# Optimization experiments

Hardware: AMD Instinct MI355X
Metric: run time of the kernel (lower is better)

Reference implementation:

```python
import jax, jax.numpy as jnp
import numpy as np

DEPTH = 16
Q_DIM = 64
V_DIM = 64
BATCH = 2048


def setup_inputs() -> dict:
    key = jax.random.key(0)
    k1, k2, k3 = jax.random.split(key, 3)
    query = jax.random.normal(k1, (BATCH, Q_DIM), dtype=jnp.float32)
    # internal-node keys: (2^depth - 1) nodes, each with 2 child keys of dim q_dim
    tree_key = jax.random.normal(k2, (2 ** DEPTH - 1, 2, Q_DIM), dtype=jnp.float32)
    # leaf values: 2^depth leaves of dim v_dim
    tree_value = jax.random.normal(k3, (2 ** DEPTH, V_DIM), dtype=jnp.float32)
    return {"query": query, "tree_key": tree_key, "tree_value": tree_value}


def _tree_attention(query, tree_key, tree_value, depth):
    # Hierarchical softmax attention over a complete binary tree.
    # At each internal node, a 2-way softmax over <query, child_key> logits
    # splits probability mass between left/right subtrees; leaf weight is the
    # product of probabilities along its root-to-leaf path.
    B = query.shape[0]
    probs = jnp.ones((B, 1), dtype=query.dtype)
    start = 0
    for d in range(depth):
        n = 2 ** d  # nodes at this level, stored contiguously at [start, start+n)
        level_keys = tree_key[start:start + n]           # (n, 2, q_dim)
        logits = jnp.einsum('bq,ncq->bnc', query, level_keys)  # (B, n, 2)
        p = jax.nn.softmax(logits, axis=-1)               # (B, n, 2)
        probs = (probs[:, :, None] * p).reshape(B, 2 * n)  # (B, 2n)
        start += n
    # weighted combination of leaf values: (B, 2^depth) @ (2^depth, v_dim)
    return probs @ tree_value


def reference(query, tree_key, tree_value):
    return _tree_attention(query, tree_key, tree_value, DEPTH)
```

## Files before the change

### kernel.cpp

```cpp
#include <hip/hip_runtime.h>

#define LOG2E 1.44269504088896f

typedef _Float16 half8  __attribute__((ext_vector_type(8)));
typedef _Float16 half4v __attribute__((ext_vector_type(4)));
typedef float    floatx4 __attribute__((ext_vector_type(4)));

#define WS_KD   0u
#define WS_VT   8388608u
#define WS_PART 16777216u

__device__ __forceinline__ floatx4 mfma16(half8 a, half8 b, floatx4 c) {
    return __builtin_amdgcn_mfma_f32_16x16x32_f16(a, b, c, 0, 0, 0);
}

__device__ __forceinline__ float sigmf(float d) {
    return __builtin_amdgcn_rcpf(1.0f + __builtin_amdgcn_exp2f(d * (-LOG2E)));
}

__device__ __forceinline__ void gl_lds16(const void* gsrc, void* ldst) {
    __builtin_amdgcn_global_load_lds(
        (const __attribute__((address_space(1))) unsigned int*)gsrc,
        (__attribute__((address_space(3))) unsigned int*)ldst,
        16, 0, 0);
}

__global__ __launch_bounds__(256)
void k_prep(const float* __restrict__ tkey, const float* __restrict__ tval,
            char* __restrict__ ws)
{
    __shared__ _Float16 sT[64 * 72];
    const int bid = blockIdx.x, tid = threadIdx.x;

    {
        const int l = tid >> 2, part = tid & 3;
        const floatx4* vp = (const floatx4*)(tval + ((size_t)bid * 64 + l) * 64) + part * 4;
        #pragma unroll
        for (int t4 = 0; t4 < 4; ++t4) {
            floatx4 f = vp[t4];
            #pragma unroll
            for (int e = 0; e < 4; ++e)
                sT[(part * 16 + t4 * 4 + e) * 72 + l] = (_Float16)f[e];
        }
    }
    __syncthreads();
    {
        const int v = tid >> 2, q4 = tid & 3;
        half8 x0 = *(const half8*)(sT + v * 72 + 16 * q4);
        half8 x1 = *(const half8*)(sT + v * 72 + 16 * q4 + 8);
        char* base = ws + WS_VT + (size_t)bid * 8192 + v * 128;
        const int swz = (v & 7) << 4;
        *(half8*)(base + ((q4 * 32)      ^ swz)) = x0;
        *(half8*)(base + ((q4 * 32 + 16) ^ swz)) = x1;
    }

    #pragma unroll
    for (int k = 0; k < 2; ++k) {
        const int gt  = bid * 512 + k * 256 + tid;
        const int rid = gt >> 3, part = gt & 7;
        const int s = rid >> 6, j = rid & 63;
        const size_t dst = (size_t)WS_KD + (size_t)s * 8192 + j * 128 + ((part * 16) ^ ((j & 7) << 4));
        half8 out;
        if (j < 63) {
            const int u = j + 1;
            const int f = 31 - __builtin_clz(u);
            const int i = u - (1 << f);
            const int gidx = ((1 << (10 + f)) - 1) + (s << f) + i;
            const floatx4* kp = (const floatx4*)(tkey + (size_t)gidx * 128) + part * 2;
            floatx4 a0 = kp[0], a1 = kp[1];
            floatx4 b0 = kp[16], b1 = kp[17];
            #pragma unroll
            for (int e = 0; e < 4; ++e) {
                out[e]     = (_Float16)(a0[e] - b0[e]);
                out[4 + e] = (_Float16)(a1[e] - b1[e]);
            }
        } else {
            #pragma unroll
            for (int e = 0; e < 8; ++e) out[e] = (_Float16)0.f;
        }
        *(half8*)(ws + dst) = out;
    }
}

__global__ __launch_bounds__(256, 2)
void k_main(const float* __restrict__ q,
            const float* __restrict__ tkey,
            const char* __restrict__ wsc,
            _Float16* __restrict__ pout)
{
    __shared__ _Float16 sA[256 * 64];
    __shared__ _Float16 sPT[256 * 72];
    __shared__ _Float16 sB[64 * 64];

    const int tid  = threadIdx.x;
    const int w    = tid >> 6;
    const int lane = tid & 63;
    const int lm   = lane & 15;
    const int quad = lane >> 4;
    const int xcd  = blockIdx.x & 7;
    const int ix   = blockIdx.x >> 3;
    const int g    = xcd * 8 + (ix >> 3);
    const int tb   = ix & 7;

    {
        const int j = tid >> 3, part = tid & 7;
        int gidx = -1;
        if (j < 6) {
            gidx = (1 << j) - 1 + (g >> (6 - j));
        } else if (j < 21) {
            const int u = j - 5;
            const int e = 31 - __builtin_clz(u);
            const int i = u - (1 << e);
            gidx = ((1 << (6 + e)) - 1) + (g << e) + i;
        }
        half8 out;
        if (gidx >= 0) {
            const floatx4* kp = (const floatx4*)(tkey + (size_t)gidx * 128) + part * 2;
            floatx4 a0 = kp[0], a1 = kp[1];
            floatx4 b0 = kp[16], b1 = kp[17];
            #pragma unroll
            for (int e = 0; e < 4; ++e) {
                out[e]     = (_Float16)(a0[e] - b0[e]);
                out[4 + e] = (_Float16)(a1[e] - b1[e]);
            }
        } else {
            #pragma unroll
            for (int e = 0; e < 8; ++e) out[e] = (_Float16)0.f;
        }
        *(half8*)(sB + j * 64 + ((part * 8) ^ ((j & 7) << 3))) = out;
    }

    {
        const int r = tid;
        const floatx4* qp = (const floatx4*)(q + (size_t)(tb * 256 + r) * 64);
        const int sw = (r & 7) << 3;
        #pragma unroll
        for (int t4 = 0; t4 < 8; ++t4) {
            floatx4 f0 = qp[2 * t4], f1 = qp[2 * t4 + 1];
            half8 hv;
            #pragma unroll
            for (int e = 0; e < 4; ++e) { hv[e] = (_Float16)f0[e]; hv[4 + e] = (_Float16)f1[e]; }
            *(half8*)(sA + r * 64 + ((t4 * 8) ^ sw)) = hv;
        }
    }
    __syncthreads();

    half8 qA[4][2];
    #pragma unroll
    for (int m = 0; m < 4; ++m) {
        const int rA = 64 * w + 16 * m + lm;
        const int sw = (lm & 7) << 3;
        #pragma unroll
        for (int kt = 0; kt < 2; ++kt)
            qA[m][kt] = *(const half8*)(sA + rA * 64 + ((kt * 32 + quad * 8) ^ sw));
    }

    {
        #pragma unroll
        for (int nt = 0; nt < 2; ++nt) {
            const int row = 16 * nt + lm;
            const int sw = (lm & 7) << 3;
            half8 bf0 = *(const half8*)(sB + row * 64 + ((quad * 8) ^ sw));
            half8 bf1 = *(const half8*)(sB + row * 64 + ((32 + quad * 8) ^ sw));
            floatx4 acc[4];
            #pragma unroll
            for (int m = 0; m < 4; ++m) {
                acc[m][0] = 0.f; acc[m][1] = 0.f; acc[m][2] = 0.f; acc[m][3] = 0.f;
                acc[m] = mfma16(bf0, qA[m][0], acc[m]);
                acc[m] = mfma16(bf1, qA[m][1], acc[m]);
            }
            #pragma unroll
            for (int m = 0; m < 4; ++m) {
                half4v ph;
                #pragma unroll
                for (int r = 0; r < 4; ++r) ph[r] = (_Float16)sigmf(acc[m][r]);
                *(half4v*)(sPT + (64 * w + 16 * m + lm) * 72 + 16 * nt + 4 * quad) = ph;
            }
        }
    }
    __syncthreads();

    const int bb = tid;
    float pref = 1.f;
    #pragma unroll
    for (int d = 0; d < 6; ++d) {
        float pv = (float)sPT[bb * 72 + d];
        pref *= ((g >> (5 - d)) & 1) ? (1.f - pv) : pv;
    }
    const float p6    = (float)sPT[bb * 72 + 6];
    const float p7_0  = (float)sPT[bb * 72 + 7],  p7_1  = (float)sPT[bb * 72 + 8];
    const float p9_0  = (float)sPT[bb * 72 + 9],  p9_1  = (float)sPT[bb * 72 + 10];
    const float p9_2  = (float)sPT[bb * 72 + 11], p9_3  = (float)sPT[bb * 72 + 12];
    const float p13_0 = (float)sPT[bb * 72 + 13], p13_1 = (float)sPT[bb * 72 + 14];
    const float p13_2 = (float)sPT[bb * 72 + 15], p13_3 = (float)sPT[bb * 72 + 16];
    const float p13_4 = (float)sPT[bb * 72 + 17], p13_5 = (float)sPT[bb * 72 + 18];
    const float p13_6 = (float)sPT[bb * 72 + 19], p13_7 = (float)sPT[bb * 72 + 20];

    floatx4 O[4][4];
    #pragma unroll
    for (int m = 0; m < 4; ++m)
        #pragma unroll
        for (int nt = 0; nt < 4; ++nt) { O[m][nt][0]=0.f; O[m][nt][1]=0.f; O[m][nt][2]=0.f; O[m][nt][3]=0.f; }

    for (int sl = 0; sl < 16; ++sl) {
        const int s = (g << 4) + sl;

        {
            const char* kd = wsc + WS_KD + (size_t)s * 8192;
            gl_lds16(kd + w * 2048 +        lane * 16, sB + w * 1024);
            gl_lds16(kd + w * 2048 + 1024 + lane * 16, sB + w * 1024 + 512);
        }
        half8 vf[4][2];
        {
            const char* vt = wsc + WS_VT + (size_t)s * 8192;
            #pragma unroll
            for (int nt = 0; nt < 4; ++nt) {
                const int row = 16 * nt + lm;
                const int swz = (lm & 7) << 4;
                #pragma unroll
                for (int kt = 0; kt < 2; ++kt)
                    vf[nt][kt] = *(const half8*)(vt + row * 128 + ((kt * 64 + quad * 16) ^ swz));
            }
        }
        __syncthreads();

        __builtin_amdgcn_s_setprio(1);
        #pragma unroll
        for (int nt = 0; nt < 4; ++nt) {
            const int row = 16 * nt + lm;
            const int sw = (lm & 7) << 3;
            half8 bf0 = *(const half8*)(sB + row * 64 + ((quad * 8) ^ sw));
            half8 bf1 = *(const half8*)(sB + row * 64 + ((32 + quad * 8) ^ sw));
            floatx4 acc[4];
            #pragma unroll
            for (int m = 0; m < 4; ++m) {
                acc[m][0] = 0.f; acc[m][1] = 0.f; acc[m][2] = 0.f; acc[m][3] = 0.f;
                acc[m] = mfma16(bf0, qA[m][0], acc[m]);
                acc[m] = mfma16(bf1, qA[m][1], acc[m]);
            }
            #pragma unroll
            for (int m = 0; m < 4; ++m) {
                half4v ph;
                #pragma unroll
                for (int r = 0; r < 4; ++r) ph[r] = (_Float16)sigmf(acc[m][r]);
                *(half4v*)(sPT + (64 * w + 16 * m + lm) * 72 + 16 * nt + 4 * quad) = ph;
            }
        }
        __builtin_amdgcn_s_setprio(0);
        __syncthreads();

        const int a0 = sl >> 3, a1 = sl >> 2, a2 = sl >> 1;
        float P0v = pref * (a0 ? (1.f - p6) : p6);
        { float v7 = a0 ? p7_1 : p7_0;                    P0v *= (a1 & 1) ? (1.f - v7) : v7; }
        { float v9 = (a1 == 0) ? p9_0 : (a1 == 1) ? p9_1 : (a1 == 2) ? p9_2 : p9_3;
                                                          P0v *= (a2 & 1) ? (1.f - v9) : v9; }
        { float vd = (a2 == 0) ? p13_0 : (a2 == 1) ? p13_1 : (a2 == 2) ? p13_2 : (a2 == 3) ? p13_3
                   : (a2 == 4) ? p13_4 : (a2 == 5) ? p13_5 : (a2 == 6) ? p13_6 : p13_7;
                                                          P0v *= (sl & 1) ? (1.f - vd) : vd; }

        half8 pr[8];
        #pragma unroll
        for (int t = 0; t < 8; ++t)
            pr[t] = *(const half8*)(sPT + bb * 72 + t * 8);
        #define PN(n) ((float)pr[(n) >> 3][(n) & 7])

        {
            #pragma unroll
            for (int qq = 0; qq < 4; ++qq) {
                float p0 = PN(0);
                float p1 = PN(1 + (qq >> 1));
                float P2 = P0v * (((qq >> 1) & 1) ? (1.f - p0) : p0)
                               * ((qq & 1) ? (1.f - p1) : p1);
                float p2 = PN(3 + qq);
                float A3[2]; A3[0] = P2 * p2; A3[1] = P2 * (1.f - p2);
                float A4[4];
                #pragma unroll
                for (int c = 0; c < 2; ++c) {
                    float pv = PN(7 + 2 * qq + c);
                    A4[2 * c] = A3[c] * pv; A4[2 * c + 1] = A3[c] * (1.f - pv);
                }
                float A5[8];
                #pragma unroll
                for (int n = 0; n < 4; ++n) {
                    float pv = PN(15 + 4 * qq + n);
                    A5[2 * n] = A4[n] * pv; A5[2 * n + 1] = A4[n] * (1.f - pv);
                }
                half8 lo, hi;
                #pragma unroll
                for (int n = 0; n < 8; ++n) {
                    float pv = PN(31 + 8 * qq + n);
                    float e0 = A5[n] * pv;
                    float e1 = A5[n] * (1.f - pv);
                    if (n < 4) { lo[2 * n] = (_Float16)e0; lo[2 * n + 1] = (_Float16)e1; }
                    else       { hi[2 * (n - 4)] = (_Float16)e0; hi[2 * (n - 4) + 1] = (_Float16)e1; }
                }
                const int sw = (bb & 7) << 3;
                *(half8*)(sA + bb * 64 + ((16 * qq)     ^ sw)) = lo;
                *(half8*)(sA + bb * 64 + ((16 * qq + 8) ^ sw)) = hi;
            }
        }
        #undef PN
        __syncthreads();

        {
            half8 af[4][2];
            #pragma unroll
            for (int m = 0; m < 4; ++m) {
                const int rA = 64 * w + 16 * m + lm;
                const int sw = (lm & 7) << 3;
                #pragma unroll
                for (int kt = 0; kt < 2; ++kt)
                    af[m][kt] = *(const half8*)(sA + rA * 64 + ((kt * 32 + quad * 8) ^ sw));
            }
            __builtin_amdgcn_s_setprio(1);
            #pragma unroll
            for (int nt = 0; nt < 4; ++nt)
                #pragma unroll
                for (int kt = 0; kt < 2; ++kt) {
                    O[0][nt] = mfma16(af[0][kt], vf[nt][kt], O[0][nt]);
                    O[1][nt] = mfma16(af[1][kt], vf[nt][kt], O[1][nt]);
                    O[2][nt] = mfma16(af[2][kt], vf[nt][kt], O[2][nt]);
                    O[3][nt] = mfma16(af[3][kt], vf[nt][kt], O[3][nt]);
                }
            __builtin_amdgcn_s_setprio(0);
        }
    }

    __syncthreads();
    #pragma unroll
    for (int m = 0; m < 4; ++m)
        #pragma unroll
        for (int nt = 0; nt < 4; ++nt)
            #pragma unroll
            for (int r = 0; r < 4; ++r) {
                const int row = 64 * w + 16 * m + 4 * quad + r;
                const int col = 16 * nt + lm;
                sA[row * 64 + (col ^ ((row & 7) << 3))] = (_Float16)O[m][nt][r];
            }
    __syncthreads();
    {
        const int row = tid;
        _Float16* dst = pout + ((size_t)g * 2048 + tb * 256 + row) * 64;
        const int sw = (row & 7) << 3;
        #pragma unroll
        for (int j = 0; j < 8; ++j)
            *(half8*)(dst + j * 8) = *(const half8*)(sA + row * 64 + ((j * 8) ^ sw));
    }
}

__global__ __launch_bounds__(256)
void k_reduce(const _Float16* __restrict__ part, float* __restrict__ outp)
{
    const int idx = blockIdx.x * 256 + threadIdx.x;
    float s0 = 0.f, s1 = 0.f, s2 = 0.f, s3 = 0.f;
    #pragma unroll 8
    for (int gg = 0; gg < 64; ++gg) {
        half4v v = *(const half4v*)(part + (size_t)gg * 131072 + (size_t)idx * 4);
        s0 += (float)v[0]; s1 += (float)v[1]; s2 += (float)v[2]; s3 += (float)v[3];
    }
    floatx4 o; o[0] = s0; o[1] = s1; o[2] = s2; o[3] = s3;
    *(floatx4*)(outp + (size_t)idx * 4) = o;
}

extern "C" void kernel_launch(void* const* d_in, const int* in_sizes, int n_in,
                              void* d_out, int out_size, void* d_ws, size_t ws_size,
                              hipStream_t stream)
{
    const float* q  = (const float*)d_in[0];
    const float* tk = (const float*)d_in[1];
    const float* tv = (const float*)d_in[2];
    float* outp = (float*)d_out;
    char*  ws   = (char*)d_ws;
    _Float16* partp = (_Float16*)(ws + WS_PART);

    k_prep  <<<dim3(1024), dim3(256), 0, stream>>>(tk, tv, ws);
    k_main  <<<dim3(512),  dim3(256), 0, stream>>>(q, tk, ws, partp);
    k_reduce<<<dim3(128),  dim3(256), 0, stream>>>(partp, outp);
}
```

Measured before the change: 166.1 us.

## Load keys and values straight into MFMA fragment layout and drop block barriers

The prep kernel now writes key differences and transposed leaf values in a fragment-major layout, so each lane loads its MFMA operands straight from global memory. This removes the global-to-LDS staging buffer for keys and the shared sB array. The per-iteration __syncthreads calls become wave-local lgkmcnt waits, since each wave now reads only the rows it wrote itself. The aim is to cut LDS traffic and block-wide barrier stalls in the inner loop. The cost is more global loads per lane, with fewer chances to hide their latency, and correctness depends on the wave-private data ownership holding.

```diff
diff --git a/kernel.cpp b/kernel.cpp
--- a/kernel.cpp
+++ b/kernel.cpp
@@ -18,11 +18,9 @@
     return __builtin_amdgcn_rcpf(1.0f + __builtin_amdgcn_exp2f(d * (-LOG2E)));
 }
 
-__device__ __forceinline__ void gl_lds16(const void* gsrc, void* ldst) {
-    __builtin_amdgcn_global_load_lds(
-        (const __attribute__((address_space(1))) unsigned int*)gsrc,
-        (__attribute__((address_space(3))) unsigned int*)ldst,
-        16, 0, 0);
+__device__ __forceinline__ void wave_lds_fence() {
+    asm volatile("s_waitcnt lgkmcnt(0)" ::: "memory");
+    __builtin_amdgcn_sched_barrier(0);
 }
 
 __global__ __launch_bounds__(256)
@@ -48,10 +46,11 @@
         const int v = tid >> 2, q4 = tid & 3;
         half8 x0 = *(const half8*)(sT + v * 72 + 16 * q4);
         half8 x1 = *(const half8*)(sT + v * 72 + 16 * q4 + 8);
-        char* base = ws + WS_VT + (size_t)bid * 8192 + v * 128;
-        const int swz = (v & 7) << 4;
-        *(half8*)(base + ((q4 * 32)      ^ swz)) = x0;
-        *(half8*)(base + ((q4 * 32 + 16) ^ swz)) = x1;
+        char* base = ws + WS_VT + (size_t)bid * 8192;
+        const int nt = v >> 4, lm = v & 15;
+        const int u0 = 2 * q4, u1 = 2 * q4 + 1;
+        *(half8*)(base + (nt * 2 + (u0 >> 2)) * 1024 + (((u0 & 3) << 4) | lm) * 16) = x0;
+        *(half8*)(base + (nt * 2 + (u1 >> 2)) * 1024 + (((u1 & 3) << 4) | lm) * 16) = x1;
     }
 
     #pragma unroll
@@ -59,7 +58,9 @@
         const int gt  = bid * 512 + k * 256 + tid;
         const int rid = gt >> 3, part = gt & 7;
         const int s = rid >> 6, j = rid & 63;
-        const size_t dst = (size_t)WS_KD + (size_t)s * 8192 + j * 128 + ((part * 16) ^ ((j & 7) << 4));
+        const size_t dst = (size_t)WS_KD + (size_t)s * 8192
+                         + ((j >> 4) * 2 + (part >> 2)) * 1024
+                         + (((part & 3) << 4) | (j & 15)) * 16;
         half8 out;
         if (j < 63) {
             const int u = j + 1;
@@ -90,7 +91,6 @@
 {
     __shared__ _Float16 sA[256 * 64];
     __shared__ _Float16 sPT[256 * 72];
-    __shared__ _Float16 sB[64 * 64];
 
     const int tid  = threadIdx.x;
     const int w    = tid >> 6;
@@ -103,6 +103,32 @@
     const int tb   = ix & 7;
 
     {
+        const int r = tid;
+        const floatx4* qp = (const floatx4*)(q + (size_t)(tb * 256 + r) * 64);
+        const int sw = (r & 7) << 3;
+        #pragma unroll
+        for (int t4 = 0; t4 < 8; ++t4) {
+            floatx4 f0 = qp[2 * t4], f1 = qp[2 * t4 + 1];
+            half8 hv;
+            #pragma unroll
+            for (int e = 0; e < 4; ++e) { hv[e] = (_Float16)f0[e]; hv[4 + e] = (_Float16)f1[e]; }
+            *(half8*)(sA + r * 64 + ((t4 * 8) ^ sw)) = hv;
+        }
+    }
+    __syncthreads();
+
+    half8 qA[4][2];
+    #pragma unroll
+    for (int m = 0; m < 4; ++m) {
+        const int rA = 64 * w + 16 * m + lm;
+        const int sw = (lm & 7) << 3;
+        #pragma unroll
+        for (int kt = 0; kt < 2; ++kt)
+            qA[m][kt] = *(const half8*)(sA + rA * 64 + ((kt * 32 + quad * 8) ^ sw));
+    }
+    __syncthreads();
+
+    {
         const int j = tid >> 3, part = tid & 7;
         int gidx = -1;
         if (j < 6) {
@@ -127,41 +153,17 @@
             #pragma unroll
             for (int e = 0; e < 8; ++e) out[e] = (_Float16)0.f;
         }
-        *(half8*)(sB + j * 64 + ((part * 8) ^ ((j & 7) << 3))) = out;
-    }
-
-    {
-        const int r = tid;
-        const floatx4* qp = (const floatx4*)(q + (size_t)(tb * 256 + r) * 64);
-        const int sw = (r & 7) << 3;
-        #pragma unroll
-        for (int t4 = 0; t4 < 8; ++t4) {
-            floatx4 f0 = qp[2 * t4], f1 = qp[2 * t4 + 1];
-            half8 hv;
-            #pragma unroll
-            for (int e = 0; e < 4; ++e) { hv[e] = (_Float16)f0[e]; hv[4 + e] = (_Float16)f1[e]; }
-            *(half8*)(sA + r * 64 + ((t4 * 8) ^ sw)) = hv;
-        }
-    }
-    __syncthreads();
-
-    half8 qA[4][2];
-    #pragma unroll
-    for (int m = 0; m < 4; ++m) {
-        const int rA = 64 * w + 16 * m + lm;
-        const int sw = (lm & 7) << 3;
-        #pragma unroll
-        for (int kt = 0; kt < 2; ++kt)
-            qA[m][kt] = *(const half8*)(sA + rA * 64 + ((kt * 32 + quad * 8) ^ sw));
-    }
+        *(half8*)(sA + j * 64 + ((part * 8) ^ ((j & 7) << 3))) = out;
+    }
+    __syncthreads();
 
     {
         #pragma unroll
         for (int nt = 0; nt < 2; ++nt) {
             const int row = 16 * nt + lm;
             const int sw = (lm & 7) << 3;
-            half8 bf0 = *(const half8*)(sB + row * 64 + ((quad * 8) ^ sw));
-            half8 bf1 = *(const half8*)(sB + row * 64 + ((32 + quad * 8) ^ sw));
+            half8 bf0 = *(const half8*)(sA + row * 64 + ((quad * 8) ^ sw));
+            half8 bf1 = *(const half8*)(sA + row * 64 + ((32 + quad * 8) ^ sw));
             floatx4 acc[4];
             #pragma unroll
             for (int m = 0; m < 4; ++m) {
@@ -205,38 +207,26 @@
     for (int sl = 0; sl < 16; ++sl) {
         const int s = (g << 4) + sl;
 
-        {
-            const char* kd = wsc + WS_KD + (size_t)s * 8192;
-            gl_lds16(kd + w * 2048 +        lane * 16, sB + w * 1024);
-            gl_lds16(kd + w * 2048 + 1024 + lane * 16, sB + w * 1024 + 512);
-        }
-        half8 vf[4][2];
-        {
-            const char* vt = wsc + WS_VT + (size_t)s * 8192;
-            #pragma unroll
-            for (int nt = 0; nt < 4; ++nt) {
-                const int row = 16 * nt + lm;
-                const int swz = (lm & 7) << 4;
-                #pragma unroll
-                for (int kt = 0; kt < 2; ++kt)
-                    vf[nt][kt] = *(const half8*)(vt + row * 128 + ((kt * 64 + quad * 16) ^ swz));
-            }
-        }
-        __syncthreads();
+        const char* kdp = wsc + WS_KD + (size_t)s * 8192;
+        const char* vtp = wsc + WS_VT + (size_t)s * 8192;
+        half8 bfr[4][2], vf[4][2];
+        #pragma unroll
+        for (int nt = 0; nt < 4; ++nt)
+            #pragma unroll
+            for (int kt = 0; kt < 2; ++kt) {
+                bfr[nt][kt] = *(const half8*)(kdp + (nt * 2 + kt) * 1024 + lane * 16);
+                vf[nt][kt]  = *(const half8*)(vtp + (nt * 2 + kt) * 1024 + lane * 16);
+            }
 
         __builtin_amdgcn_s_setprio(1);
         #pragma unroll
         for (int nt = 0; nt < 4; ++nt) {
-            const int row = 16 * nt + lm;
-            const int sw = (lm & 7) << 3;
-            half8 bf0 = *(const half8*)(sB + row * 64 + ((quad * 8) ^ sw));
-            half8 bf1 = *(const half8*)(sB + row * 64 + ((32 + quad * 8) ^ sw));
             floatx4 acc[4];
             #pragma unroll
             for (int m = 0; m < 4; ++m) {
                 acc[m][0] = 0.f; acc[m][1] = 0.f; acc[m][2] = 0.f; acc[m][3] = 0.f;
-                acc[m] = mfma16(bf0, qA[m][0], acc[m]);
-                acc[m] = mfma16(bf1, qA[m][1], acc[m]);
+                acc[m] = mfma16(bfr[nt][0], qA[m][0], acc[m]);
+                acc[m] = mfma16(bfr[nt][1], qA[m][1], acc[m]);
             }
             #pragma unroll
             for (int m = 0; m < 4; ++m) {
@@ -247,7 +237,7 @@
             }
         }
         __builtin_amdgcn_s_setprio(0);
-        __syncthreads();
+        wave_lds_fence();
 
         const int a0 = sl >> 3, a1 = sl >> 2, a2 = sl >> 1;
         float P0v = pref * (a0 ? (1.f - p6) : p6);
@@ -264,43 +254,41 @@
             pr[t] = *(const half8*)(sPT + bb * 72 + t * 8);
         #define PN(n) ((float)pr[(n) >> 3][(n) & 7])
 
-        {
-            #pragma unroll
-            for (int qq = 0; qq < 4; ++qq) {
-                float p0 = PN(0);
-                float p1 = PN(1 + (qq >> 1));
-                float P2 = P0v * (((qq >> 1) & 1) ? (1.f - p0) : p0)
-                               * ((qq & 1) ? (1.f - p1) : p1);
-                float p2 = PN(3 + qq);
-                float A3[2]; A3[0] = P2 * p2; A3[1] = P2 * (1.f - p2);
-                float A4[4];
-                #pragma unroll
-                for (int c = 0; c < 2; ++c) {
-                    float pv = PN(7 + 2 * qq + c);
-                    A4[2 * c] = A3[c] * pv; A4[2 * c + 1] = A3[c] * (1.f - pv);
-                }
-                float A5[8];
-                #pragma unroll
-                for (int n = 0; n < 4; ++n) {
-                    float pv = PN(15 + 4 * qq + n);
-                    A5[2 * n] = A4[n] * pv; A5[2 * n + 1] = A4[n] * (1.f - pv);
-                }
-                half8 lo, hi;
-                #pragma unroll
-                for (int n = 0; n < 8; ++n) {
-                    float pv = PN(31 + 8 * qq + n);
-                    float e0 = A5[n] * pv;
-                    float e1 = A5[n] * (1.f - pv);
-                    if (n < 4) { lo[2 * n] = (_Float16)e0; lo[2 * n + 1] = (_Float16)e1; }
-                    else       { hi[2 * (n - 4)] = (_Float16)e0; hi[2 * (n - 4) + 1] = (_Float16)e1; }
-                }
-                const int sw = (bb & 7) << 3;
-                *(half8*)(sA + bb * 64 + ((16 * qq)     ^ sw)) = lo;
-                *(half8*)(sA + bb * 64 + ((16 * qq + 8) ^ sw)) = hi;
-            }
+        #pragma unroll
+        for (int qq = 0; qq < 4; ++qq) {
+            float p0 = PN(0);
+            float p1 = PN(1 + (qq >> 1));
+            float P2 = P0v * (((qq >> 1) & 1) ? (1.f - p0) : p0)
+                           * ((qq & 1) ? (1.f - p1) : p1);
+            float p2 = PN(3 + qq);
+            float A3[2]; A3[0] = P2 * p2; A3[1] = P2 * (1.f - p2);
+            float A4[4];
+            #pragma unroll
+            for (int c = 0; c < 2; ++c) {
+                float pv = PN(7 + 2 * qq + c);
+                A4[2 * c] = A3[c] * pv; A4[2 * c + 1] = A3[c] * (1.f - pv);
+            }
+            float A5[8];
+            #pragma unroll
+            for (int n = 0; n < 4; ++n) {
+                float pv = PN(15 + 4 * qq + n);
+                A5[2 * n] = A4[n] * pv; A5[2 * n + 1] = A4[n] * (1.f - pv);
+            }
+            half8 lo, hi;
+            #pragma unroll
+            for (int n = 0; n < 8; ++n) {
+                float pv = PN(31 + 8 * qq + n);
+                float e0 = A5[n] * pv;
+                float e1 = A5[n] * (1.f - pv);
+                if (n < 4) { lo[2 * n] = (_Float16)e0; lo[2 * n + 1] = (_Float16)e1; }
+                else       { hi[2 * (n - 4)] = (_Float16)e0; hi[2 * (n - 4) + 1] = (_Float16)e1; }
+            }
+            const int sw = (bb & 7) << 3;
+            *(half8*)(sA + bb * 64 + ((16 * qq)     ^ sw)) = lo;
+            *(half8*)(sA + bb * 64 + ((16 * qq + 8) ^ sw)) = hi;
         }
         #undef PN
-        __syncthreads();
+        wave_lds_fence();
 
         {
             half8 af[4][2];
```

Result: no change. 164.7 us (-0.8%).
